# Performance work log

Measured on AMD Instinct MI355X. Metric: run time of the kernel, lower is better.

Reference implementation:

```python
import jax, jax.numpy as jnp
import numpy as np

USERNUM = 8192
ITEMNUM = 8192
DIM = 256
EPS_NORM = 1e-8   # torch.cosine_similarity default eps
CLAMP_MIN = 1e-6
CLAMP_MAX = 1.0


def setup_inputs() -> dict:
    key = jax.random.key(0)
    ks = jax.random.split(key, 12)
    N = USERNUM + ITEMNUM
    s = 1.0 / np.sqrt(DIM)
    return {
        "A": jax.random.uniform(ks[0], (N, N), dtype=jnp.float32) * (2.0 / N),
        "features": jax.random.normal(ks[1], (N, DIM), dtype=jnp.float32),
        "Wg": jax.random.normal(ks[2], (DIM, DIM), dtype=jnp.float32) * s,
        "bg": jnp.zeros((DIM,), dtype=jnp.float32),
        "uW1": jax.random.normal(ks[3], (DIM, DIM), dtype=jnp.float32) * s,
        "ub1": jnp.zeros((DIM,), dtype=jnp.float32),
        "uW2": jax.random.normal(ks[4], (DIM, DIM), dtype=jnp.float32) * s,
        "ub2": jnp.zeros((DIM,), dtype=jnp.float32),
        "iW1": jax.random.normal(ks[5], (DIM, DIM), dtype=jnp.float32) * s,
        "ib1": jnp.zeros((DIM,), dtype=jnp.float32),
        "iW2": jax.random.normal(ks[6], (DIM, DIM), dtype=jnp.float32) * s,
        "ib2": jnp.zeros((DIM,), dtype=jnp.float32),
    }


def _mlp(h, W1, b1, W2, b2):
    return jax.nn.relu(h @ W1 + b1) @ W2 + b2


def reference(A, features, Wg, bg, uW1, ub1, uW2, ub2, iW1, ib1, iW2, ib2):
    # GCN layer: relu(A @ X @ W + b)  -> [N, DIM]
    x = jax.nn.relu((A @ features) @ Wg + bg)
    user = x[:USERNUM]
    item = x[USERNUM:]
    u = _mlp(user, uW1, ub1, uW2, ub2)   # [usernum, DIM]
    it = _mlp(item, iW1, ib1, iW2, ib2)  # [itemnum, DIM]
    # Fused L2-normalize + GEMM replaces the per-row cosine_similarity loop.
    un = u / jnp.maximum(jnp.linalg.norm(u, axis=1, keepdims=True), EPS_NORM)
    itn = it / jnp.maximum(jnp.linalg.norm(it, axis=1, keepdims=True), EPS_NORM)
    sim = un @ itn.T                      # [usernum, itemnum]
    return jnp.clip(sim, CLAMP_MIN, CLAMP_MAX)
```

## Files before the change

### kernel.cpp

```cpp
#include <hip/hip_runtime.h>
#include <hip/hip_bf16.h>

using f32x4 = __attribute__((ext_vector_type(4))) float;
using s16x8 = __attribute__((ext_vector_type(8))) short;
using i32x4 = __attribute__((ext_vector_type(4))) int;

#define NTOT 16384
#define NUSER 8192
#define DIM 256

__device__ __forceinline__ unsigned short f2bf(float f) {
  union { float f; unsigned u; } v; v.f = f;
  unsigned r = v.u + 0x7FFFu + ((v.u >> 16) & 1u);
  return (unsigned short)(r >> 16);
}

__device__ __forceinline__ unsigned pack2bf(float x, float y) {
  float2 t; t.x = x; t.y = y;
  __hip_bfloat162 h = __float22bfloat162_rn(t);
  union { __hip_bfloat162 h; unsigned u; } cv; cv.h = h;
  return cv.u;
}

__device__ __forceinline__ void gload_lds16(const void* g, void* l) {
  __builtin_amdgcn_global_load_lds(
      (const __attribute__((address_space(1))) unsigned int*)g,
      (__attribute__((address_space(3))) unsigned int*)l, 16, 0, 0);
}

__global__ __launch_bounds__(256) void transpose_cvt(const float* __restrict__ src,
                                                     unsigned short* __restrict__ dst,
                                                     int K, int N) {
  __shared__ float tile[64][65];
  const int k0 = blockIdx.x * 64, n0 = blockIdx.y * 64;
  const int t = threadIdx.x;
#pragma unroll
  for (int i = 0; i < 16; i++) {
    int idx = i * 256 + t, r = idx >> 6, c = idx & 63;
    tile[r][c] = src[(size_t)(k0 + r) * N + n0 + c];
  }
  __syncthreads();
#pragma unroll
  for (int i = 0; i < 16; i++) {
    int idx = i * 256 + t, r = idx >> 6, c = idx & 63;
    dst[(size_t)(n0 + r) * K + k0 + c] = f2bf(tile[c][r]);
  }
}

__global__ __launch_bounds__(256) void transpose_w5(const float* __restrict__ w0,
                                                    const float* __restrict__ w1,
                                                    const float* __restrict__ w2,
                                                    const float* __restrict__ w3,
                                                    const float* __restrict__ w4,
                                                    unsigned short* __restrict__ dstbase) {
  __shared__ float tile[64][65];
  const float* srcs[5] = {w0, w1, w2, w3, w4};
  const float* src = srcs[blockIdx.z];
  unsigned short* dst = dstbase + (size_t)blockIdx.z * 65536;
  const int k0 = blockIdx.x * 64, n0 = blockIdx.y * 64;
  const int t = threadIdx.x;
#pragma unroll
  for (int i = 0; i < 16; i++) {
    int idx = i * 256 + t, r = idx >> 6, c = idx & 63;
    tile[r][c] = src[(size_t)(k0 + r) * 256 + n0 + c];
  }
  __syncthreads();
#pragma unroll
  for (int i = 0; i < 16; i++) {
    int idx = i * 256 + t, r = idx >> 6, c = idx & 63;
    dst[(size_t)(n0 + r) * 256 + k0 + c] = f2bf(tile[c][r]);
  }
}

__global__ __launch_bounds__(512) void gemm1(const float* __restrict__ A,
                                             const unsigned short* __restrict__ Ft,
                                             float* __restrict__ F1p) {
  __shared__ char smem[144 * 1024];
  char* const Ab0 = smem;
  char* const Ab1 = smem + 16 * 1024;
  char* const Ab2 = smem + 32 * 1024;
  char* const Bb0 = smem + 48 * 1024;
  char* const Bb1 = smem + 80 * 1024;
  char* const Bb2 = smem + 112 * 1024;

  const int tid = threadIdx.x;
  const int l = tid & 63, w = tid >> 6;
  const int wm = w >> 2, wn = w & 3;
  const int lr = l & 15, lk = l >> 4;

  const int lin = blockIdx.x;
  const int xcd = lin & 7, slot = lin >> 3;
  const int ks = xcd >> 2;
  const int mblk = (xcd & 3) * 32 + slot;
  const int m0 = mblk * 128;
  const size_t ks0 = (size_t)ks * 8192;
  float* out = F1p + (size_t)ks * NTOT * DIM;

  const int arow = tid >> 4, ac16 = tid & 15;
  const float* asrc = A + (size_t)(m0 + arow) * NTOT + ks0 + ac16 * 4;
  int aoff[4];
#pragma unroll
  for (int j = 0; j < 4; j++) {
    int r = j * 32 + arow;
    aoff[j] = r * 128 + ((ac16 * 8) ^ ((r & 7) << 4));
  }

  const int brin = l >> 3;
  const int bldso = w * 4096;
  const char* bsrc = (const char*)Ft + (size_t)(w * 32 + brin) * (NTOT * 2) +
                     ks0 * 2 + (((l & 7) * 16) ^ (brin << 4));

  f32x4 zero = {0.f, 0.f, 0.f, 0.f};
  f32x4 acc[4][4];
#pragma unroll
  for (int i = 0; i < 4; i++)
#pragma unroll
    for (int j = 0; j < 4; j++) acc[i][j] = zero;

  struct AQuad { f32x4 v[4]; };
  AQuad av0, av1, av2;

  auto issueB = [&](int t, char* Bb) {
#pragma unroll
    for (int i = 0; i < 4; i++)
      gload_lds16(bsrc + (size_t)i * 8 * (NTOT * 2) + t * 128,
                  Bb + bldso + i * 1024);
  };
  auto loadA = [&](int t, AQuad& s) {
#pragma unroll
    for (int j = 0; j < 4; j++)
      s.v[j] = __builtin_nontemporal_load(
          (const f32x4*)(asrc + (size_t)j * 32 * NTOT + t * 64));
  };
  auto writeA = [&](const AQuad& s, char* Ab) {
#pragma unroll
    for (int j = 0; j < 4; j++) {
      unsigned lo = pack2bf(s.v[j].x, s.v[j].y);
      unsigned hi = pack2bf(s.v[j].z, s.v[j].w);
      *(unsigned long long*)(Ab + aoff[j]) =
          (unsigned long long)lo | ((unsigned long long)hi << 32);
    }
  };
  auto compute = [&](const char* Ab, const char* Bb) {
#pragma unroll
    for (int kh = 0; kh < 2; kh++) {
      s16x8 af[4], bf[4];
#pragma unroll
      for (int mt = 0; mt < 4; mt++) {
        int r = wm * 64 + mt * 16 + lr;
        int off = r * 128 + ((kh * 64 + lk * 16) ^ ((r & 7) << 4));
        af[mt] = *(const s16x8*)(Ab + off);
      }
#pragma unroll
      for (int nt = 0; nt < 4; nt++) {
        int n = wn * 64 + nt * 16 + lr;
        int off = n * 128 + ((kh * 64 + lk * 16) ^ ((n & 7) << 4));
        bf[nt] = *(const s16x8*)(Bb + off);
      }
#pragma unroll
      for (int mt = 0; mt < 4; mt++)
#pragma unroll
        for (int nt = 0; nt < 4; nt++)
          acc[mt][nt] = __builtin_amdgcn_mfma_f32_16x16x32_bf16(af[mt], bf[nt],
                                                                acc[mt][nt], 0, 0, 0);
    }
  };

#define STEP_BAR(N)                                                \
  asm volatile("s_waitcnt vmcnt(" #N ") lgkmcnt(0)" ::: "memory"); \
  __builtin_amdgcn_s_barrier();                                    \
  __builtin_amdgcn_sched_barrier(0);

  issueB(0, Bb0);
  loadA(0, av0);
  issueB(1, Bb1);
  loadA(1, av1);
  writeA(av0, Ab0);
  STEP_BAR(8)

  for (int t = 0; t < 126; t += 3) {
    issueB(t + 2, Bb2);
    loadA(t + 2, av2);
    compute(Ab0, Bb0);
    writeA(av1, Ab1);
    STEP_BAR(8)
    issueB(t + 3, Bb0);
    loadA(t + 3, av0);
    compute(Ab1, Bb1);
    writeA(av2, Ab2);
    STEP_BAR(8)
    issueB(t + 4, Bb1);
    loadA(t + 4, av1);
    compute(Ab2, Bb2);
    writeA(av0, Ab0);
    STEP_BAR(8)
  }
  compute(Ab0, Bb0);
  writeA(av1, Ab1);
  STEP_BAR(0)
  compute(Ab1, Bb1);
#undef STEP_BAR

#pragma unroll
  for (int mt = 0; mt < 4; mt++) {
    int rbase = m0 + wm * 64 + mt * 16 + lk * 4;
#pragma unroll
    for (int nt = 0; nt < 4; nt++) {
      int c = wn * 64 + nt * 16 + lr;
#pragma unroll
      for (int j = 0; j < 4; j++)
        __builtin_nontemporal_store(acc[mt][nt][j],
                                    out + (size_t)(rbase + j) * DIM + c);
    }
  }
}

__global__ __launch_bounds__(512) void mlp_fused(const float* __restrict__ P,
                                                 const unsigned short* __restrict__ WgT,
                                                 const float* __restrict__ bg,
                                                 const unsigned short* __restrict__ uW1T,
                                                 const unsigned short* __restrict__ iW1T,
                                                 const float* __restrict__ ub1,
                                                 const float* __restrict__ ib1,
                                                 const unsigned short* __restrict__ uW2T,
                                                 const unsigned short* __restrict__ iW2T,
                                                 const float* __restrict__ ub2,
                                                 const float* __restrict__ ib2,
                                                 unsigned short* __restrict__ un) {
  __shared__ char smem[96 * 1024];
  char* const Xa = smem;
  char* const Xb = smem + 32 * 1024;
  char* const Bb = smem + 64 * 1024;
  __shared__ float rs[64][4];

  const int tid = threadIdx.x, l = tid & 63, w = tid >> 6;
  const int wm = w >> 2, wn = w & 3;
  const int m0 = blockIdx.x * 64;
  const unsigned short* W1 = (m0 < NUSER) ? uW1T : iW1T;
  const float* b1 = (m0 < NUSER) ? ub1 : ib1;
  const unsigned short* W2 = (m0 < NUSER) ? uW2T : iW2T;
  const float* b2 = (m0 < NUSER) ? ub2 : ib2;
  const int arow = tid >> 4, ac4 = tid & 15;
  const int bn = tid >> 3, bg_ = tid & 7;
  const int lr = l & 15, lk = l >> 4;

#pragma unroll
  for (int step = 0; step < 4; step++)
#pragma unroll
    for (int i = 0; i < 2; i++) {
      int r = i * 32 + arow;
      size_t gi = (size_t)(m0 + r) * DIM + step * 64 + ac4 * 4;
      f32x4 v = *(const f32x4*)(P + gi);
      v += *(const f32x4*)(P + (size_t)NTOT * DIM + gi);
      unsigned lo = pack2bf(v.x, v.y);
      unsigned hi = pack2bf(v.z, v.w);
      int off = r * 512 + ((step * 128 + ac4 * 8) ^ ((r & 7) << 4));
      *(unsigned long long*)(Xa + off) =
          (unsigned long long)lo | ((unsigned long long)hi << 32);
    }

  f32x4 zero = {0.f, 0.f, 0.f, 0.f};
  f32x4 acc[2][4];

  auto phase = [&](const char* Alds, const unsigned short* WT) {
#pragma unroll
    for (int i = 0; i < 2; i++)
#pragma unroll
      for (int j = 0; j < 4; j++) acc[i][j] = zero;
    for (int step = 0; step < 4; step++) {
#pragma unroll
      for (int i = 0; i < 4; i++) {
        int n = i * 64 + bn;
        i32x4 v = *(const i32x4*)(WT + (size_t)n * DIM + step * 64 + bg_ * 8);
        int off = (n * 128 + bg_ * 16) ^ ((n & 7) << 4);
        *(i32x4*)(Bb + off) = v;
      }
      __syncthreads();
#pragma unroll
      for (int kh = 0; kh < 2; kh++) {
        s16x8 af[2], bfr[4];
#pragma unroll
        for (int mt = 0; mt < 2; mt++) {
          int r = wm * 32 + mt * 16 + lr;
          int off = r * 512 + ((step * 128 + kh * 64 + lk * 16) ^ ((r & 7) << 4));
          af[mt] = *(const s16x8*)(Alds + off);
        }
#pragma unroll
        for (int nt = 0; nt < 4; nt++) {
          int n = wn * 64 + nt * 16 + lr;
          int off = (n * 128 + kh * 64 + lk * 16) ^ ((n & 7) << 4);
          bfr[nt] = *(const s16x8*)(Bb + off);
        }
#pragma unroll
        for (int mt = 0; mt < 2; mt++)
#pragma unroll
          for (int nt = 0; nt < 4; nt++)
            acc[mt][nt] = __builtin_amdgcn_mfma_f32_16x16x32_bf16(af[mt], bfr[nt],
                                                                  acc[mt][nt], 0, 0, 0);
      }
      __syncthreads();
    }
  };
  auto reluToLds = [&](const float* bias, char* dst) {
#pragma unroll
    for (int nt = 0; nt < 4; nt++) {
      int c = wn * 64 + nt * 16 + lr;
      float b = bias[c];
#pragma unroll
      for (int mt = 0; mt < 2; mt++) {
        int rbase = wm * 32 + mt * 16 + lk * 4;
#pragma unroll
        for (int j = 0; j < 4; j++) {
          float v = fmaxf(acc[mt][nt][j] + b, 0.f);
          int row = rbase + j;
          int off = row * 512 + ((c * 2) ^ ((row & 7) << 4));
          *(unsigned short*)(dst + off) = f2bf(v);
        }
      }
    }
  };

  __syncthreads();
  phase(Xa, WgT);
  reluToLds(bg, Xb);
  __syncthreads();
  phase(Xb, W1);
  reluToLds(b1, Xa);
  __syncthreads();
  phase(Xa, W2);

  float uval[2][4][4];
  float p[2][4];
#pragma unroll
  for (int mt = 0; mt < 2; mt++)
#pragma unroll
    for (int j = 0; j < 4; j++) p[mt][j] = 0.f;
#pragma unroll
  for (int nt = 0; nt < 4; nt++) {
    int c = wn * 64 + nt * 16 + lr;
    float b = b2[c];
#pragma unroll
    for (int mt = 0; mt < 2; mt++)
#pragma unroll
      for (int j = 0; j < 4; j++) {
        float v = acc[mt][nt][j] + b;
        uval[mt][nt][j] = v;
        p[mt][j] += v * v;
      }
  }
#pragma unroll
  for (int d = 1; d < 16; d <<= 1)
#pragma unroll
    for (int mt = 0; mt < 2; mt++)
#pragma unroll
      for (int j = 0; j < 4; j++) p[mt][j] += __shfl_xor(p[mt][j], d, 64);
  if (lr == 0) {
#pragma unroll
    for (int mt = 0; mt < 2; mt++)
#pragma unroll
      for (int j = 0; j < 4; j++) rs[wm * 32 + mt * 16 + lk * 4 + j][wn] = p[mt][j];
  }
  __syncthreads();
#pragma unroll
  for (int mt = 0; mt < 2; mt++) {
    int rl = wm * 32 + mt * 16 + lk * 4;
#pragma unroll
    for (int j = 0; j < 4; j++) {
      float tot = rs[rl + j][0] + rs[rl + j][1] + rs[rl + j][2] + rs[rl + j][3];
      float inv = 1.f / fmaxf(sqrtf(tot), 1e-8f);
#pragma unroll
      for (int nt = 0; nt < 4; nt++) {
        int c = wn * 64 + nt * 16 + lr;
        un[(size_t)(m0 + rl + j) * DIM + c] = f2bf(uval[mt][nt][j] * inv);
      }
    }
  }
}

__global__ __launch_bounds__(512) void simk(const unsigned short* __restrict__ UN,
                                            float* __restrict__ out) {
  __shared__ char smem[128 * 1024];
  char* Ab = smem;
  char* Bb = smem + 64 * 1024;
  const int tid = threadIdx.x, l = tid & 63, w = tid >> 6;
  const int wm = w >> 2, wn = w & 3;
  const int lin = blockIdx.x + (blockIdx.y << 6);
  const int xcd = lin & 7, slot = lin >> 3;
  const int nblk = xcd * 8 + (slot & 7);
  const int mblk = slot >> 3;
  const int m0 = mblk * 128, n0 = nblk * 128;
  const int lr = l & 15, lk = l >> 4;
  const int sr = tid >> 5, sg = tid & 31;

#pragma unroll
  for (int i = 0; i < 8; i++) {
    int r = i * 16 + sr;
    i32x4 va = *(const i32x4*)(UN + (size_t)(m0 + r) * DIM + sg * 8);
    i32x4 vb = *(const i32x4*)(UN + (size_t)(NUSER + n0 + r) * DIM + sg * 8);
    int off = (r * 512 + sg * 16) ^ ((r & 7) << 4);
    *(i32x4*)(Ab + off) = va;
    *(i32x4*)(Bb + off) = vb;
  }
  __syncthreads();

  f32x4 zero = {0.f, 0.f, 0.f, 0.f};
  f32x4 acc[4][2];
#pragma unroll
  for (int i = 0; i < 4; i++)
#pragma unroll
    for (int j = 0; j < 2; j++) acc[i][j] = zero;

#pragma unroll
  for (int ks = 0; ks < 8; ks++) {
    s16x8 af[4], bfr[2];
#pragma unroll
    for (int mt = 0; mt < 4; mt++) {
      int r = wm * 64 + mt * 16 + lr;
      int off = (r * 512 + ks * 64 + lk * 16) ^ ((r & 7) << 4);
      af[mt] = *(const s16x8*)(Ab + off);
    }
#pragma unroll
    for (int nt = 0; nt < 2; nt++) {
      int n = wn * 32 + nt * 16 + lr;
      int off = (n * 512 + ks * 64 + lk * 16) ^ ((n & 7) << 4);
      bfr[nt] = *(const s16x8*)(Bb + off);
    }
#pragma unroll
    for (int mt = 0; mt < 4; mt++)
#pragma unroll
      for (int nt = 0; nt < 2; nt++)
        acc[mt][nt] = __builtin_amdgcn_mfma_f32_16x16x32_bf16(af[mt], bfr[nt],
                                                              acc[mt][nt], 0, 0, 0);
  }

#pragma unroll
  for (int mt = 0; mt < 4; mt++) {
    int rbase = m0 + wm * 64 + mt * 16 + lk * 4;
#pragma unroll
    for (int nt = 0; nt < 2; nt++) {
      int c = n0 + wn * 32 + nt * 16 + lr;
#pragma unroll
      for (int j = 0; j < 4; j++) {
        float v = fminf(fmaxf(acc[mt][nt][j], 1e-6f), 1.0f);
        __builtin_nontemporal_store(v, out + (size_t)(rbase + j) * 8192 + c);
      }
    }
  }
}

extern "C" void kernel_launch(void* const* d_in, const int* in_sizes, int n_in,
                              void* d_out, int out_size, void* d_ws, size_t ws_size,
                              hipStream_t stream) {
  const float* A    = (const float*)d_in[0];
  const float* feat = (const float*)d_in[1];
  const float* Wg   = (const float*)d_in[2];
  const float* bg   = (const float*)d_in[3];
  const float* uW1  = (const float*)d_in[4];
  const float* ub1  = (const float*)d_in[5];
  const float* uW2  = (const float*)d_in[6];
  const float* ub2  = (const float*)d_in[7];
  const float* iW1  = (const float*)d_in[8];
  const float* ib1  = (const float*)d_in[9];
  const float* iW2  = (const float*)d_in[10];
  const float* ib2  = (const float*)d_in[11];
  float* out = (float*)d_out;
  char* ob = (char*)d_out;

  float*          F1p  = (float*)(ob + 0);
  unsigned short* Ft   = (unsigned short*)(ob + 33554432);
  unsigned short* WT5  = (unsigned short*)(ob + 41943040);
  unsigned short* WgT  = WT5;
  unsigned short* uW1T = WT5 + 1 * 65536;
  unsigned short* uW2T = WT5 + 2 * 65536;
  unsigned short* iW1T = WT5 + 3 * 65536;
  unsigned short* iW2T = WT5 + 4 * 65536;
  unsigned short* UN   = (unsigned short*)d_ws;

  transpose_cvt<<<dim3(256, 4), 256, 0, stream>>>(feat, Ft, NTOT, DIM);
  transpose_w5<<<dim3(4, 4, 5), 256, 0, stream>>>(Wg, uW1, uW2, iW1, iW2, WT5);

  gemm1<<<dim3(256), 512, 0, stream>>>(A, Ft, F1p);
  mlp_fused<<<dim3(256), 512, 0, stream>>>(F1p, WgT, bg, uW1T, iW1T, ub1, ib1,
                                           uW2T, iW2T, ub2, ib2, UN);
  simk<<<dim3(64, 64), 512, 0, stream>>>(UN, out);
}
```

Baseline: 320.7 us.

## Restructure gemm1 pipeline to double-buffer wider A chunks with separate B stages

Result: slower. 362.0 us (+12.9%).

```diff
diff --git a/kernel.cpp b/kernel.cpp
--- a/kernel.cpp
+++ b/kernel.cpp
@@ -72,16 +72,16 @@
   }
 }
 
+struct AChunk { f32x4 v[8]; };
+
 __global__ __launch_bounds__(512) void gemm1(const float* __restrict__ A,
                                              const unsigned short* __restrict__ Ft,
                                              float* __restrict__ F1p) {
-  __shared__ char smem[144 * 1024];
+  __shared__ char smem[128 * 1024];
   char* const Ab0 = smem;
-  char* const Ab1 = smem + 16 * 1024;
-  char* const Ab2 = smem + 32 * 1024;
-  char* const Bb0 = smem + 48 * 1024;
-  char* const Bb1 = smem + 80 * 1024;
-  char* const Bb2 = smem + 112 * 1024;
+  char* const Ab1 = smem + 32 * 1024;
+  char* const Bb0 = smem + 64 * 1024;
+  char* const Bb1 = smem + 96 * 1024;
 
   const int tid = threadIdx.x;
   const int l = tid & 63, w = tid >> 6;
@@ -98,11 +98,13 @@
 
   const int arow = tid >> 4, ac16 = tid & 15;
   const float* asrc = A + (size_t)(m0 + arow) * NTOT + ks0 + ac16 * 4;
-  int aoff[4];
+  int aoffb[4][2];
 #pragma unroll
   for (int j = 0; j < 4; j++) {
     int r = j * 32 + arow;
-    aoff[j] = r * 128 + ((ac16 * 8) ^ ((r & 7) << 4));
+#pragma unroll
+    for (int c = 0; c < 2; c++)
+      aoffb[j][c] = r * 256 + ((c * 128 + ac16 * 8) ^ ((r & 7) << 4));
   }
 
   const int brin = l >> 3;
@@ -117,8 +119,7 @@
 #pragma unroll
     for (int j = 0; j < 4; j++) acc[i][j] = zero;
 
-  struct AQuad { f32x4 v[4]; };
-  AQuad av0, av1, av2;
+  AChunk avP, avQ;
 
   auto issueB = [&](int t, char* Bb) {
 #pragma unroll
@@ -126,29 +127,33 @@
       gload_lds16(bsrc + (size_t)i * 8 * (NTOT * 2) + t * 128,
                   Bb + bldso + i * 1024);
   };
-  auto loadA = [&](int t, AQuad& s) {
+  auto issueA = [&](int u, AChunk& s) {
 #pragma unroll
     for (int j = 0; j < 4; j++)
-      s.v[j] = __builtin_nontemporal_load(
-          (const f32x4*)(asrc + (size_t)j * 32 * NTOT + t * 64));
-  };
-  auto writeA = [&](const AQuad& s, char* Ab) {
-#pragma unroll
-    for (int j = 0; j < 4; j++) {
-      unsigned lo = pack2bf(s.v[j].x, s.v[j].y);
-      unsigned hi = pack2bf(s.v[j].z, s.v[j].w);
-      *(unsigned long long*)(Ab + aoff[j]) =
-          (unsigned long long)lo | ((unsigned long long)hi << 32);
-    }
-  };
-  auto compute = [&](const char* Ab, const char* Bb) {
+#pragma unroll
+      for (int c = 0; c < 2; c++)
+        s.v[j * 2 + c] = __builtin_nontemporal_load(
+            (const f32x4*)(asrc + (size_t)j * 32 * NTOT + u * 128 + c * 64));
+  };
+  auto writeA = [&](const AChunk& s, char* Ab) {
+#pragma unroll
+    for (int j = 0; j < 4; j++)
+#pragma unroll
+      for (int c = 0; c < 2; c++) {
+        unsigned lo = pack2bf(s.v[j * 2 + c].x, s.v[j * 2 + c].y);
+        unsigned hi = pack2bf(s.v[j * 2 + c].z, s.v[j * 2 + c].w);
+        *(unsigned long long*)(Ab + aoffb[j][c]) =
+            (unsigned long long)lo | ((unsigned long long)hi << 32);
+      }
+  };
+  auto computeStep = [&](const char* Ab, int h, const char* Bb) {
 #pragma unroll
     for (int kh = 0; kh < 2; kh++) {
       s16x8 af[4], bf[4];
 #pragma unroll
       for (int mt = 0; mt < 4; mt++) {
         int r = wm * 64 + mt * 16 + lr;
-        int off = r * 128 + ((kh * 64 + lk * 16) ^ ((r & 7) << 4));
+        int off = r * 256 + ((h * 128 + kh * 64 + lk * 16) ^ ((r & 7) << 4));
         af[mt] = *(const s16x8*)(Ab + off);
       }
 #pragma unroll
@@ -166,40 +171,47 @@
     }
   };
 
-#define STEP_BAR(N)                                                \
+#define BAR_V(N)                                                   \
   asm volatile("s_waitcnt vmcnt(" #N ") lgkmcnt(0)" ::: "memory"); \
   __builtin_amdgcn_s_barrier();                                    \
   __builtin_amdgcn_sched_barrier(0);
 
+  issueA(0, avP);
   issueB(0, Bb0);
-  loadA(0, av0);
-  issueB(1, Bb1);
-  loadA(1, av1);
-  writeA(av0, Ab0);
-  STEP_BAR(8)
-
-  for (int t = 0; t < 126; t += 3) {
-    issueB(t + 2, Bb2);
-    loadA(t + 2, av2);
-    compute(Ab0, Bb0);
-    writeA(av1, Ab1);
-    STEP_BAR(8)
-    issueB(t + 3, Bb0);
-    loadA(t + 3, av0);
-    compute(Ab1, Bb1);
-    writeA(av2, Ab2);
-    STEP_BAR(8)
-    issueB(t + 4, Bb1);
-    loadA(t + 4, av1);
-    compute(Ab2, Bb2);
-    writeA(av0, Ab0);
-    STEP_BAR(8)
-  }
-  compute(Ab0, Bb0);
-  writeA(av1, Ab1);
-  STEP_BAR(0)
-  compute(Ab1, Bb1);
-#undef STEP_BAR
+  writeA(avP, Ab0);
+  issueA(1, avQ);
+  BAR_V(8)
+
+  for (int i = 0; i < 31; i++) {
+    issueB(4 * i + 1, Bb1);
+    computeStep(Ab0, 0, Bb0);
+    writeA(avQ, Ab1);
+    BAR_V(0)
+    issueB(4 * i + 2, Bb0);
+    issueA(2 * i + 2, avP);
+    computeStep(Ab0, 1, Bb1);
+    BAR_V(8)
+    issueB(4 * i + 3, Bb1);
+    computeStep(Ab1, 0, Bb0);
+    writeA(avP, Ab0);
+    BAR_V(0)
+    issueB(4 * i + 4, Bb0);
+    issueA(2 * i + 3, avQ);
+    computeStep(Ab1, 1, Bb1);
+    BAR_V(8)
+  }
+  issueB(125, Bb1);
+  computeStep(Ab0, 0, Bb0);
+  writeA(avQ, Ab1);
+  BAR_V(0)
+  issueB(126, Bb0);
+  computeStep(Ab0, 1, Bb1);
+  BAR_V(0)
+  issueB(127, Bb1);
+  computeStep(Ab1, 0, Bb0);
+  BAR_V(0)
+  computeStep(Ab1, 1, Bb1);
+#undef BAR_V
 
 #pragma unroll
   for (int mt = 0; mt < 4; mt++) {
```
